# Kernel tuning notes

Measured on AMD Instinct MI355X. Metric: run time of the kernel, lower is better.

Reference implementation:

```python
import jax, jax.numpy as jnp
import numpy as np

N = 100000   # nodes
E = 1600000  # edges
IN = 128     # in_channels
H = 96       # hidden
G = 512      # graphs in batch


def setup_inputs() -> dict:
    key = jax.random.key(0)
    ks = jax.random.split(key, 11)
    x = jax.random.normal(ks[0], (N, IN), jnp.float32)
    edge_index = jax.random.randint(ks[1], (2, E), 0, N)
    batch = jnp.sort(jax.random.randint(ks[2], (N,), 0, G))
    def lin(k, fan_in, fan_out):
        lim = 1.0 / np.sqrt(fan_in)
        kw, kb = jax.random.split(k)
        W = jax.random.uniform(kw, (fan_in, fan_out), jnp.float32, -lim, lim)
        b = jax.random.uniform(kb, (fan_out,), jnp.float32, -lim, lim)
        return W, b
    W1, b1 = lin(ks[3], IN, H)
    W2, b2 = lin(ks[4], H, H)
    Wn, bn = lin(ks[5], 2 * H, 1)
    Wg, bg = lin(ks[6], 4 * H, 1)
    return dict(x=x, edge_index=edge_index, batch=batch,
                W1=W1, b1=b1, W2=W2, b2=b2, Wn=Wn, bn=bn, Wg=Wg, bg=bg)


def reference(x, edge_index, batch, W1, b1, W2, b2, Wn, bn, Wg, bg):
    # --- GCN normalization with self-loops: D^-1/2 (A+I) D^-1/2 ---
    loops = jnp.arange(N)
    src = jnp.concatenate([edge_index[0], loops])  # [E+N]
    dst = jnp.concatenate([edge_index[1], loops])
    deg = jax.ops.segment_sum(jnp.ones_like(dst, jnp.float32), dst, num_segments=N)
    dis = jnp.where(deg > 0, jax.lax.rsqrt(jnp.maximum(deg, 1.0)), 0.0)
    norm = dis[src] * dis[dst]  # [E+N]

    def gcn_conv(h, W, b):
        hw = h @ W                                # transform first (smaller msgs)
        msg = hw[src] * norm[:, None]             # gather + scale  [E+N, H]
        return jax.ops.segment_sum(msg, dst, num_segments=N) + b

    h1 = jax.nn.relu(gcn_conv(x, W1, b1))         # dropout: eval no-op
    h2 = jax.nn.relu(gcn_conv(h1, W2, b2))
    h = jnp.concatenate([h1, h2], axis=1)         # [N, 2H]

    node_logits = (h @ Wn + bn).reshape(-1)       # [N]

    cnt = jax.ops.segment_sum(jnp.ones((N,), jnp.float32), batch, num_segments=G)
    meanp = jax.ops.segment_sum(h, batch, num_segments=G) / jnp.maximum(cnt, 1.0)[:, None]
    maxp = jax.ops.segment_max(h, batch, num_segments=G)
    maxp = jnp.where(cnt[:, None] > 0, maxp, 0.0)
    pooled = jnp.concatenate([meanp, maxp], axis=1)  # [G, 4H]

    graph_logits = (pooled @ Wg + bg).reshape(-1)    # [G]
    return graph_logits, node_logits
```

## Files before the change

### kernel.cpp

```cpp
#include <hip/hip_runtime.h>
#include <hip/hip_fp16.h>

#define NN 100000
#define NE 1600000
#define INC 128
#define HID 96
#define NG 512

#define GEMM1_BLOCKS 1563
#define G2_BLOCKS 1563

#define BK_SHIFT 8
#define BK_SIZE 256
#define NBK 391
#define A_EPB 4096
#define A_BLOCKS 391

typedef _Float16 half8 __attribute__((ext_vector_type(8)));
typedef float f32x4 __attribute__((ext_vector_type(4)));

__global__ __launch_bounds__(256) void k_pack_a1(const int* __restrict__ dst,
                                                 int* __restrict__ histAB,
                                                 const float* __restrict__ W1,
                                                 const float* __restrict__ W2,
                                                 __half* __restrict__ W1frag,
                                                 __half* __restrict__ W2frag) {
    const int tid = threadIdx.x;
    if (blockIdx.x < A_BLOCKS) {
        __shared__ int cnt[NBK];
        int ab = blockIdx.x;
        for (int i = tid; i < NBK; i += 256) cnt[i] = 0;
        __syncthreads();
        int e0 = ab * A_EPB;
#pragma unroll 4
        for (int q = 0; q < A_EPB / 256; ++q) {
            int e = e0 + q * 256 + tid;
            if (e < NE) atomicAdd(&cnt[dst[e] >> BK_SHIFT], 1);
        }
        __syncthreads();
        for (int i = tid; i < NBK; i += 256) histAB[ab * NBK + i] = cnt[i];
        return;
    }
    int p = (blockIdx.x - A_BLOCKS) * 256 + tid;
    if (p < 1536) {
        int kc = p / 384;
        int rem = p - kc * 384;
        int ct = rem >> 6;
        int l = rem & 63;
#pragma unroll
        for (int i = 0; i < 8; ++i) {
            int k = kc * 32 + ((l >> 4) << 3) + i;
            int c = ct * 16 + (l & 15);
            W1frag[p * 8 + i] = __float2half(W1[k * HID + c]);
        }
    } else {
        int q = p - 1536;
        if (q >= 1152) return;
        int kc = q / 384;
        int rem = q - kc * 384;
        int ct = rem >> 6;
        int l = rem & 63;
#pragma unroll
        for (int i = 0; i < 8; ++i) {
            int k = kc * 32 + ((l >> 4) << 3) + i;
            int c = ct * 16 + (l & 15);
            W2frag[q * 8 + i] = __float2half(W2[k * HID + c]);
        }
    }
}

__global__ __launch_bounds__(512) void k_scanS(int* __restrict__ histAB, int* __restrict__ boff) {
    __shared__ int tot[512];
    int t = threadIdx.x;
    int run = 0;
    if (t < NBK) {
        for (int blk = 0; blk < A_BLOCKS; ++blk) {
            int idx = blk * NBK + t;
            int v = histAB[idx];
            histAB[idx] = run;
            run += v;
        }
    }
    tot[t] = (t < NBK) ? run : 0;
    __syncthreads();
    for (int ofs = 1; ofs < 512; ofs <<= 1) {
        int v = (t >= ofs) ? tot[t - ofs] : 0;
        __syncthreads();
        tot[t] += v;
        __syncthreads();
    }
    if (t == 0) boff[0] = 0;
    if (t < NBK) boff[t + 1] = tot[t];
}

__global__ __launch_bounds__(256) void k_gemm1_a3(
        const float* __restrict__ X, const __half* __restrict__ W1frag,
        __half* __restrict__ Yh,
        const int* __restrict__ src, const int* __restrict__ dst,
        const int* __restrict__ boff, const int* __restrict__ histAB,
        unsigned* __restrict__ tmp) {
    __shared__ __half w1s[12288];
    const int tid = threadIdx.x;

    if (blockIdx.x < A_BLOCKS) {
        int* base = (int*)w1s;
        int* lcnt = base + NBK;
        int ab = blockIdx.x;
        for (int i = tid; i < NBK; i += 256) {
            base[i] = boff[i] + histAB[ab * NBK + i];
            lcnt[i] = 0;
        }
        __syncthreads();
        int e0 = ab * A_EPB;
#pragma unroll 4
        for (int q = 0; q < A_EPB / 256; ++q) {
            int e = e0 + q * 256 + tid;
            if (e < NE) {
                int d = dst[e];
                int bk = d >> BK_SHIFT;
                int lp = atomicAdd(&lcnt[bk], 1);
                tmp[base[bk] + lp] = (unsigned)src[e] | ((unsigned)(d & (BK_SIZE - 1)) << 17);
            }
        }
        return;
    }

    {
        half8* d8 = (half8*)w1s;
        const half8* s8 = (const half8*)W1frag;
        for (int i = tid; i < 1536; i += 256) d8[i] = s8[i];
    }
    __syncthreads();
    const int w = tid >> 6;
    const int l = tid & 63;
    const int row0 = (blockIdx.x - A_BLOCKS) * 64 + w * 16;
    int arow = row0 + (l & 15);
    if (arow >= NN) arow = NN - 1;
    f32x4 acc[6] = {};
#pragma unroll
    for (int kc = 0; kc < 4; ++kc) {
        const float* xp = &X[(size_t)arow * INC + kc * 32 + ((l >> 4) << 3)];
        float4 xa = *(const float4*)xp;
        float4 xb = *(const float4*)(xp + 4);
        half8 a;
        a[0] = (_Float16)xa.x; a[1] = (_Float16)xa.y;
        a[2] = (_Float16)xa.z; a[3] = (_Float16)xa.w;
        a[4] = (_Float16)xb.x; a[5] = (_Float16)xb.y;
        a[6] = (_Float16)xb.z; a[7] = (_Float16)xb.w;
#pragma unroll
        for (int ct = 0; ct < 6; ++ct) {
            half8 b = *(const half8*)&w1s[((kc * 6 + ct) * 64 + l) * 8];
            acc[ct] = __builtin_amdgcn_mfma_f32_16x16x32_f16(a, b, acc[ct], 0, 0, 0);
        }
    }
    const int orow = row0 + ((l >> 4) << 2);
    const int col = l & 15;
#pragma unroll
    for (int ct = 0; ct < 6; ++ct)
#pragma unroll
        for (int i = 0; i < 4; ++i) {
            int r = orow + i;
            if (r < NN) Yh[(size_t)r * HID + ct * 16 + col] = __float2half(acc[ct][i]);
        }
}

__global__ __launch_bounds__(256) void k_B1(const unsigned* __restrict__ tmp,
                                            const int* __restrict__ boff,
                                            int* __restrict__ off, float* __restrict__ dis) {
    __shared__ int cnt[BK_SIZE];
    __shared__ int psum[256];
    const int t = threadIdx.x;
    const int b = blockIdx.x;
    const int nb = b << BK_SHIFT;
    const int rbeg = boff[b], rend = boff[b + 1];
    cnt[t] = 0;
    __syncthreads();
    for (int e = rbeg + t; e < rend; e += 256) {
        unsigned u = tmp[e];
        atomicAdd(&cnt[u >> 17], 1);
    }
    __syncthreads();
    int c = cnt[t];
    psum[t] = c;
    __syncthreads();
    for (int ofs = 1; ofs < 256; ofs <<= 1) {
        int v = (t >= ofs) ? psum[t - ofs] : 0;
        __syncthreads();
        psum[t] += v;
        __syncthreads();
    }
    int node = nb + t;
    if (node < NN) {
        off[node] = rbeg + psum[t] - c;
        dis[node] = rsqrtf((float)(c + 1));
    }
    if (b == NBK - 1 && t == 0) off[NN] = rend;
}

__global__ __launch_bounds__(256) void k_B2(const unsigned* __restrict__ tmp,
                                            const int* __restrict__ boff,
                                            const int* __restrict__ off,
                                            const float* __restrict__ dis,
                                            int2* __restrict__ ssrcw) {
    __shared__ int cnt[BK_SIZE];
    const int t = threadIdx.x;
    const int b = blockIdx.x;
    const int nb = b << BK_SHIFT;
    const int rbeg = boff[b], rend = boff[b + 1];
    cnt[t] = 0;
    __syncthreads();
    for (int e = rbeg + t; e < rend; e += 256) {
        unsigned u = tmp[e];
        int s = (int)(u & 0x1FFFFu);
        int dl = (int)(u >> 17);
        int d = nb + dl;
        int pos = off[d] + atomicAdd(&cnt[dl], 1);
        float w = dis[s] * dis[d];
        ssrcw[pos] = make_int2(s, __float_as_int(w));
    }
}

__global__ __launch_bounds__(256) void k_gemm2(const __half* __restrict__ Xh,
                                               const __half* __restrict__ W2frag,
                                               __half* __restrict__ Yh) {
    __shared__ __half w2s[9216];
    const int tid = threadIdx.x;
    {
        half8* d8 = (half8*)w2s;
        const half8* s8 = (const half8*)W2frag;
        for (int i = tid; i < 1152; i += 256) d8[i] = s8[i];
    }
    __syncthreads();
    const int w = tid >> 6;
    const int l = tid & 63;
    const int row0 = blockIdx.x * 64 + w * 16;
    int arow = row0 + (l & 15);
    if (arow >= NN) arow = NN - 1;
    f32x4 acc[6] = {};
#pragma unroll
    for (int kc = 0; kc < 3; ++kc) {
        half8 a = *(const half8*)&Xh[(size_t)arow * HID + kc * 32 + ((l >> 4) << 3)];
#pragma unroll
        for (int ct = 0; ct < 6; ++ct) {
            half8 b = *(const half8*)&w2s[((kc * 6 + ct) * 64 + l) * 8];
            acc[ct] = __builtin_amdgcn_mfma_f32_16x16x32_f16(a, b, acc[ct], 0, 0, 0);
        }
    }
    const int orow = row0 + ((l >> 4) << 2);
    const int col = l & 15;
#pragma unroll
    for (int ct = 0; ct < 6; ++ct)
#pragma unroll
        for (int i = 0; i < 4; ++i) {
            int r = orow + i;
            if (r < NN) Yh[(size_t)r * HID + ct * 16 + col] = __float2half(acc[ct][i]);
        }
}

template <int B>
__device__ __forceinline__ void agg_batch(const __half* __restrict__ Ah,
                                          const int2* __restrict__ ssrcw, int j, int t,
                                          float& a0x, float& a0y, float& a1x, float& a1y,
                                          float& a2x, float& a2y) {
    int2 e[B];
#pragma unroll
    for (int q = 0; q < B; ++q) e[q] = ssrcw[j + q];
    float w[B];
    const __half2* ap[B];
#pragma unroll
    for (int q = 0; q < B; ++q) {
        w[q] = __int_as_float(e[q].y);
        ap[q] = (const __half2*)(Ah + (size_t)e[q].x * HID);
    }
    __half2 g0[B], g1[B], g2[B];
#pragma unroll
    for (int q = 0; q < B; ++q) {
        g0[q] = ap[q][t];
        g1[q] = ap[q][t + 16];
        g2[q] = ap[q][t + 32];
    }
#pragma unroll
    for (int q = 0; q < B; ++q) {
        float2 f0 = __half22float2(g0[q]);
        float2 f1 = __half22float2(g1[q]);
        float2 f2 = __half22float2(g2[q]);
        a0x += f0.x * w[q]; a0y += f0.y * w[q];
        a1x += f1.x * w[q]; a1y += f1.y * w[q];
        a2x += f2.x * w[q]; a2y += f2.y * w[q];
    }
}

template <int PHASE>
__global__ __launch_bounds__(256) void k_agg(const __half* __restrict__ Ah,
                                             const int2* __restrict__ ssrcw,
                                             const int* __restrict__ off,
                                             const float* __restrict__ dis,
                                             const float* __restrict__ bias,
                                             const float* __restrict__ Wn,
                                             const float* __restrict__ bn,
                                             __half* __restrict__ outh,
                                             float* __restrict__ nodeOut) {
    int gid = blockIdx.x * blockDim.x + threadIdx.x;
    int d = gid >> 4;
    int t = gid & 15;
    if (d >= NN) return;
    const int beg = off[d], end = off[d + 1];
    const float dd = dis[d];
    const __half2* ad2 = (const __half2*)(Ah + (size_t)d * HID);
    float2 s0 = __half22float2(ad2[t]);
    float2 s1 = __half22float2(ad2[t + 16]);
    float2 s2 = __half22float2(ad2[t + 32]);
    const float dd2 = dd * dd;
    float a0x = s0.x * dd2, a0y = s0.y * dd2;
    float a1x = s1.x * dd2, a1y = s1.y * dd2;
    float a2x = s2.x * dd2, a2y = s2.y * dd2;
    int j = beg;
    for (; j + 11 < end; j += 12)
        agg_batch<12>(Ah, ssrcw, j, t, a0x, a0y, a1x, a1y, a2x, a2y);
    for (; j + 3 < end; j += 4)
        agg_batch<4>(Ah, ssrcw, j, t, a0x, a0y, a1x, a1y, a2x, a2y);
    for (; j < end; ++j) {
        int2 e0 = ssrcw[j];
        float w0 = __int_as_float(e0.y);
        const __half2* a0 = (const __half2*)(Ah + (size_t)e0.x * HID);
        float2 f0 = __half22float2(a0[t]);
        float2 f1 = __half22float2(a0[t + 16]);
        float2 f2 = __half22float2(a0[t + 32]);
        a0x += f0.x * w0; a0y += f0.y * w0;
        a1x += f1.x * w0; a1y += f1.y * w0;
        a2x += f2.x * w0; a2y += f2.y * w0;
    }
    const float2* b2p = (const float2*)bias;
    float2 b0 = b2p[t], b1 = b2p[t + 16], b2 = b2p[t + 32];
    float h0x = fmaxf(a0x + b0.x, 0.f), h0y = fmaxf(a0y + b0.y, 0.f);
    float h1x = fmaxf(a1x + b1.x, 0.f), h1y = fmaxf(a1y + b1.y, 0.f);
    float h2x = fmaxf(a2x + b2.x, 0.f), h2y = fmaxf(a2y + b2.y, 0.f);
    __half2* o2 = (__half2*)(outh + (size_t)d * HID);
    o2[t]      = __floats2half2_rn(h0x, h0y);
    o2[t + 16] = __floats2half2_rn(h1x, h1y);
    o2[t + 32] = __floats2half2_rn(h2x, h2y);

    const int woff = (PHASE == 1) ? 0 : 96;
    const float2* wn2 = (const float2*)(Wn + woff);
    float2 w0v = wn2[t], w1v = wn2[t + 16], w2v = wn2[t + 32];
    float partial = h0x * w0v.x + h0y * w0v.y + h1x * w1v.x + h1y * w1v.y +
                    h2x * w2v.x + h2y * w2v.y;
#pragma unroll
    for (int m = 8; m; m >>= 1) partial += __shfl_down(partial, m, 16);
    if (t == 0) {
        if (PHASE == 1) nodeOut[d] = partial + bn[0];
        else            nodeOut[d] += partial;
    }
}

__global__ __launch_bounds__(768) void k_pool(const __half* __restrict__ h1,
                                              const __half* __restrict__ h2,
                                              const int* __restrict__ batch,
                                              const float* __restrict__ Wg,
                                              const float* __restrict__ bg,
                                              float* __restrict__ out) {
    int g = blockIdx.x;
    int tid = threadIdx.x;
    int way = tid / 192;
    int f = tid - way * 192;

    int lo = 0, hi = NN;
    while (lo < hi) { int mid = (lo + hi) >> 1; if (batch[mid] < g) lo = mid + 1; else hi = mid; }
    int start = lo;
    hi = NN;
    while (lo < hi) { int mid = (lo + hi) >> 1; if (batch[mid] < g + 1) lo = mid + 1; else hi = mid; }
    int end = lo;

    const __half* hsrc = (f < HID) ? h1 : h2;
    int ff = (f < HID) ? f : f - HID;
    float sum = 0.f, mx = 0.f;
    int n = start + way;
    for (; n + 4 < end; n += 8) {
        float v0 = __half2float(hsrc[(size_t)n * HID + ff]);
        float v1 = __half2float(hsrc[(size_t)(n + 4) * HID + ff]);
        sum += v0 + v1;
        mx = fmaxf(mx, fmaxf(v0, v1));
    }
    if (n < end) {
        float v0 = __half2float(hsrc[(size_t)n * HID + ff]);
        sum += v0;
        mx = fmaxf(mx, v0);
    }
    __shared__ float rsum[4][192];
    __shared__ float rmax[4][192];
    rsum[way][f] = sum;
    rmax[way][f] = mx;
    __syncthreads();
    if (way == 0) {
        sum = rsum[0][f] + rsum[1][f] + rsum[2][f] + rsum[3][f];
        mx = fmaxf(fmaxf(rmax[0][f], rmax[1][f]), fmaxf(rmax[2][f], rmax[3][f]));
        float cnt = (float)(end - start);
        float mean = sum / fmaxf(cnt, 1.0f);
        rsum[0][f] = mean * Wg[f] + mx * Wg[192 + f];
    }
    __syncthreads();
    if (tid < 64) {
        float acc = rsum[0][tid] + rsum[0][tid + 64] + rsum[0][tid + 128];
#pragma unroll
        for (int m = 32; m; m >>= 1) acc += __shfl_down(acc, m, 64);
        if (tid == 0) out[g] = acc + bg[0];
    }
}

extern "C" void kernel_launch(void* const* d_in, const int* in_sizes, int n_in,
                              void* d_out, int out_size, void* d_ws, size_t ws_size,
                              hipStream_t stream) {
    const float* x    = (const float*)d_in[0];
    const int*   ei   = (const int*)d_in[1];
    const int*   srcp = ei;
    const int*   dstp = ei + NE;
    const int*   batch = (const int*)d_in[2];
    const float* W1 = (const float*)d_in[3];
    const float* b1 = (const float*)d_in[4];
    const float* W2 = (const float*)d_in[5];
    const float* b2 = (const float*)d_in[6];
    const float* Wn = (const float*)d_in[7];
    const float* bn = (const float*)d_in[8];
    const float* Wg = (const float*)d_in[9];
    const float* bg = (const float*)d_in[10];
    float* out = (float*)d_out;

    char* p = (char*)d_ws;
    auto alloc = [&](size_t bytes) {
        char* r = p;
        p += (bytes + 255) & ~(size_t)255;
        return (void*)r;
    };
    float*    dis    = (float*)alloc(NN * 4);
    int*      off    = (int*)alloc((NN + 1) * 4);
    int*      boff   = (int*)alloc((NBK + 1) * 4);
    int*      histAB = (int*)alloc((size_t)A_BLOCKS * NBK * 4);
    unsigned* tmp    = (unsigned*)alloc((size_t)NE * 4);
    int2*     ssrcw  = (int2*)alloc((size_t)NE * 8);
    __half*   Ah     = (__half*)alloc((size_t)NN * HID * 2);
    __half*   H1h    = (__half*)alloc((size_t)NN * HID * 2);
    __half*   H2h    = (__half*)alloc((size_t)NN * HID * 2);
    __half*   W1frag = (__half*)alloc(12288 * 2);
    __half*   W2frag = (__half*)alloc(9216 * 2);

    const int TPB = 256;

    k_pack_a1<<<A_BLOCKS + 11, TPB, 0, stream>>>(dstp, histAB, W1, W2, W1frag, W2frag);
    k_scanS<<<1, 512, 0, stream>>>(histAB, boff);
    k_gemm1_a3<<<A_BLOCKS + GEMM1_BLOCKS, 256, 0, stream>>>(
        x, W1frag, Ah, srcp, dstp, boff, histAB, tmp);
    k_B1<<<NBK, 256, 0, stream>>>(tmp, boff, off, dis);
    k_B2<<<NBK, 256, 0, stream>>>(tmp, boff, off, dis, ssrcw);

    const int aggThreads = NN * 16;
    float* nodeOut = out + NG;

    k_agg<1><<<(aggThreads + TPB - 1) / TPB, TPB, 0, stream>>>(Ah, ssrcw, off, dis, b1, Wn, bn, H1h, nodeOut);

    k_gemm2<<<G2_BLOCKS, 256, 0, stream>>>(H1h, W2frag, Ah);

    k_agg<2><<<(aggThreads + TPB - 1) / TPB, TPB, 0, stream>>>(Ah, ssrcw, off, dis, b2, Wn, bn, H2h, nodeOut);

    k_pool<<<NG, 768, 0, stream>>>(H1h, H2h, batch, Wg, bg, out);
}
```

Before: 238.2 us.

## Fuse layer-2 GEMM into aggregation by aggregating before transforming

Layer 2 now aggregates H1 directly and then multiplies the aggregated row by W2 inside the aggregation kernel. The per-node accumulators are staged in shared memory, and W2 is held in LDS as plain fp16. This drops the separate MFMA gemm2 kernel along with its write and re-read of the transformed feature buffer. In exchange every node does a 96x96 scalar FP32 mat-vec read from LDS, and each block needs about 24KB of dynamic LDS plus a block barrier, which may reduce occupancy of this latency-bound gather kernel.

```diff
diff --git a/kernel.cpp b/kernel.cpp
--- a/kernel.cpp
+++ b/kernel.cpp
@@ -8,7 +8,6 @@
 #define NG 512
 
 #define GEMM1_BLOCKS 1563
-#define G2_BLOCKS 1563
 
 #define BK_SHIFT 8
 #define BK_SIZE 256
@@ -24,7 +23,7 @@
                                                  const float* __restrict__ W1,
                                                  const float* __restrict__ W2,
                                                  __half* __restrict__ W1frag,
-                                                 __half* __restrict__ W2frag) {
+                                                 __half* __restrict__ W2h) {
     const int tid = threadIdx.x;
     if (blockIdx.x < A_BLOCKS) {
         __shared__ int cnt[NBK];
@@ -56,16 +55,8 @@
     } else {
         int q = p - 1536;
         if (q >= 1152) return;
-        int kc = q / 384;
-        int rem = q - kc * 384;
-        int ct = rem >> 6;
-        int l = rem & 63;
-#pragma unroll
-        for (int i = 0; i < 8; ++i) {
-            int k = kc * 32 + ((l >> 4) << 3) + i;
-            int c = ct * 16 + (l & 15);
-            W2frag[q * 8 + i] = __float2half(W2[k * HID + c]);
-        }
+#pragma unroll
+        for (int i = 0; i < 8; ++i) W2h[q * 8 + i] = __float2half(W2[q * 8 + i]);
     }
 }
 
@@ -220,43 +211,6 @@
     }
 }
 
-__global__ __launch_bounds__(256) void k_gemm2(const __half* __restrict__ Xh,
-                                               const __half* __restrict__ W2frag,
-                                               __half* __restrict__ Yh) {
-    __shared__ __half w2s[9216];
-    const int tid = threadIdx.x;
-    {
-        half8* d8 = (half8*)w2s;
-        const half8* s8 = (const half8*)W2frag;
-        for (int i = tid; i < 1152; i += 256) d8[i] = s8[i];
-    }
-    __syncthreads();
-    const int w = tid >> 6;
-    const int l = tid & 63;
-    const int row0 = blockIdx.x * 64 + w * 16;
-    int arow = row0 + (l & 15);
-    if (arow >= NN) arow = NN - 1;
-    f32x4 acc[6] = {};
-#pragma unroll
-    for (int kc = 0; kc < 3; ++kc) {
-        half8 a = *(const half8*)&Xh[(size_t)arow * HID + kc * 32 + ((l >> 4) << 3)];
-#pragma unroll
-        for (int ct = 0; ct < 6; ++ct) {
-            half8 b = *(const half8*)&w2s[((kc * 6 + ct) * 64 + l) * 8];
-            acc[ct] = __builtin_amdgcn_mfma_f32_16x16x32_f16(a, b, acc[ct], 0, 0, 0);
-        }
-    }
-    const int orow = row0 + ((l >> 4) << 2);
-    const int col = l & 15;
-#pragma unroll
-    for (int ct = 0; ct < 6; ++ct)
-#pragma unroll
-        for (int i = 0; i < 4; ++i) {
-            int r = orow + i;
-            if (r < NN) Yh[(size_t)r * HID + ct * 16 + col] = __float2half(acc[ct][i]);
-        }
-}
-
 template <int B>
 __device__ __forceinline__ void agg_batch(const __half* __restrict__ Ah,
                                           const int2* __restrict__ ssrcw, int j, int t,
@@ -298,12 +252,21 @@
                                              const float* __restrict__ bias,
                                              const float* __restrict__ Wn,
                                              const float* __restrict__ bn,
+                                             const __half* __restrict__ W2h,
                                              __half* __restrict__ outh,
                                              float* __restrict__ nodeOut) {
+    extern __shared__ char smem[];
     int gid = blockIdx.x * blockDim.x + threadIdx.x;
     int d = gid >> 4;
     int t = gid & 15;
+
+    if (PHASE == 2) {
+        half8* d8 = (half8*)smem;
+        const half8* s8 = (const half8*)W2h;
+        for (int i = threadIdx.x; i < 1152; i += 256) d8[i] = s8[i];
+    }
     if (d >= NN) return;
+
     const int beg = off[d], end = off[d + 1];
     const float dd = dis[d];
     const __half2* ad2 = (const __half2*)(Ah + (size_t)d * HID);
@@ -330,26 +293,59 @@
         a1x += f1.x * w0; a1y += f1.y * w0;
         a2x += f2.x * w0; a2y += f2.y * w0;
     }
-    const float2* b2p = (const float2*)bias;
-    float2 b0 = b2p[t], b1 = b2p[t + 16], b2 = b2p[t + 32];
-    float h0x = fmaxf(a0x + b0.x, 0.f), h0y = fmaxf(a0y + b0.y, 0.f);
-    float h1x = fmaxf(a1x + b1.x, 0.f), h1y = fmaxf(a1y + b1.y, 0.f);
-    float h2x = fmaxf(a2x + b2.x, 0.f), h2y = fmaxf(a2y + b2.y, 0.f);
-    __half2* o2 = (__half2*)(outh + (size_t)d * HID);
-    o2[t]      = __floats2half2_rn(h0x, h0y);
-    o2[t + 16] = __floats2half2_rn(h1x, h1y);
-    o2[t + 32] = __floats2half2_rn(h2x, h2y);
-
-    const int woff = (PHASE == 1) ? 0 : 96;
-    const float2* wn2 = (const float2*)(Wn + woff);
-    float2 w0v = wn2[t], w1v = wn2[t + 16], w2v = wn2[t + 32];
-    float partial = h0x * w0v.x + h0y * w0v.y + h1x * w1v.x + h1y * w1v.y +
-                    h2x * w2v.x + h2y * w2v.y;
-#pragma unroll
-    for (int m = 8; m; m >>= 1) partial += __shfl_down(partial, m, 16);
-    if (t == 0) {
-        if (PHASE == 1) nodeOut[d] = partial + bn[0];
-        else            nodeOut[d] += partial;
+
+    if (PHASE == 1) {
+        const float2* b2p = (const float2*)bias;
+        float2 b0 = b2p[t], b1 = b2p[t + 16], b2 = b2p[t + 32];
+        float h0x = fmaxf(a0x + b0.x, 0.f), h0y = fmaxf(a0y + b0.y, 0.f);
+        float h1x = fmaxf(a1x + b1.x, 0.f), h1y = fmaxf(a1y + b1.y, 0.f);
+        float h2x = fmaxf(a2x + b2.x, 0.f), h2y = fmaxf(a2y + b2.y, 0.f);
+        __half2* o2 = (__half2*)(outh + (size_t)d * HID);
+        o2[t]      = __floats2half2_rn(h0x, h0y);
+        o2[t + 16] = __floats2half2_rn(h1x, h1y);
+        o2[t + 32] = __floats2half2_rn(h2x, h2y);
+        const float2* wn2 = (const float2*)Wn;
+        float2 w0v = wn2[t], w1v = wn2[t + 16], w2v = wn2[t + 32];
+        float partial = h0x * w0v.x + h0y * w0v.y + h1x * w1v.x + h1y * w1v.y +
+                        h2x * w2v.x + h2y * w2v.y;
+#pragma unroll
+        for (int m = 8; m; m >>= 1) partial += __shfl_down(partial, m, 16);
+        if (t == 0) nodeOut[d] = partial + bn[0];
+    } else {
+        float* Mg = (float*)(smem + 18432) + (threadIdx.x >> 4) * 100;
+        Mg[2 * t] = a0x;      Mg[2 * t + 1] = a0y;
+        Mg[32 + 2 * t] = a1x; Mg[33 + 2 * t] = a1y;
+        Mg[64 + 2 * t] = a2x; Mg[65 + 2 * t] = a2y;
+        __syncthreads();
+        const __half2* w2s2 = (const __half2*)smem;
+        float y0x = 0, y0y = 0, y1x = 0, y1y = 0, y2x = 0, y2y = 0;
+#pragma unroll 8
+        for (int k = 0; k < 96; ++k) {
+            float m = Mg[k];
+            __half2 wa = w2s2[k * 48 + 3 * t];
+            __half2 wb = w2s2[k * 48 + 3 * t + 1];
+            __half2 wc = w2s2[k * 48 + 3 * t + 2];
+            float2 fa = __half22float2(wa), fb = __half22float2(wb), fc = __half22float2(wc);
+            y0x += m * fa.x; y0y += m * fa.y;
+            y1x += m * fb.x; y1y += m * fb.y;
+            y2x += m * fc.x; y2y += m * fc.y;
+        }
+        const float2* b2p = (const float2*)bias;
+        float2 B0 = b2p[3 * t], B1 = b2p[3 * t + 1], B2v = b2p[3 * t + 2];
+        float h0x = fmaxf(y0x + B0.x, 0.f), h0y = fmaxf(y0y + B0.y, 0.f);
+        float h1x = fmaxf(y1x + B1.x, 0.f), h1y = fmaxf(y1y + B1.y, 0.f);
+        float h2x = fmaxf(y2x + B2v.x, 0.f), h2y = fmaxf(y2y + B2v.y, 0.f);
+        __half2* o2 = (__half2*)(outh + (size_t)d * HID);
+        o2[3 * t]     = __floats2half2_rn(h0x, h0y);
+        o2[3 * t + 1] = __floats2half2_rn(h1x, h1y);
+        o2[3 * t + 2] = __floats2half2_rn(h2x, h2y);
+        const float2* wn2 = (const float2*)(Wn + 96);
+        float2 w0v = wn2[3 * t], w1v = wn2[3 * t + 1], w2v = wn2[3 * t + 2];
+        float partial = h0x * w0v.x + h0y * w0v.y + h1x * w1v.x + h1y * w1v.y +
+                        h2x * w2v.x + h2y * w2v.y;
+#pragma unroll
+        for (int m = 8; m; m >>= 1) partial += __shfl_down(partial, m, 16);
+        if (t == 0) nodeOut[d] += partial;
     }
 }
 
@@ -441,11 +437,11 @@
     __half*   H1h    = (__half*)alloc((size_t)NN * HID * 2);
     __half*   H2h    = (__half*)alloc((size_t)NN * HID * 2);
     __half*   W1frag = (__half*)alloc(12288 * 2);
-    __half*   W2frag = (__half*)alloc(9216 * 2);
+    __half*   W2h    = (__half*)alloc(9216 * 2);
 
     const int TPB = 256;
 
-    k_pack_a1<<<A_BLOCKS + 11, TPB, 0, stream>>>(dstp, histAB, W1, W2, W1frag, W2frag);
+    k_pack_a1<<<A_BLOCKS + 11, TPB, 0, stream>>>(dstp, histAB, W1, W2, W1frag, W2h);
     k_scanS<<<1, 512, 0, stream>>>(histAB, boff);
     k_gemm1_a3<<<A_BLOCKS + GEMM1_BLOCKS, 256, 0, stream>>>(
         x, W1frag, Ah, srcp, dstp, boff, histAB, tmp);
@@ -453,13 +449,12 @@
     k_B2<<<NBK, 256, 0, stream>>>(tmp, boff, off, dis, ssrcw);
 
     const int aggThreads = NN * 16;
+    const int aggBlocks = aggThreads / TPB;
     float* nodeOut = out + NG;
 
-    k_agg<1><<<(aggThreads + TPB - 1) / TPB, TPB, 0, stream>>>(Ah, ssrcw, off, dis, b1, Wn, bn, H1h, nodeOut);
-
-    k_gemm2<<<G2_BLOCKS, 256, 0, stream>>>(H1h, W2frag, Ah);
-
-    k_agg<2><<<(aggThreads + TPB - 1) / TPB, TPB, 0, stream>>>(Ah, ssrcw, off, dis, b2, Wn, bn, H2h, nodeOut);
+    k_agg<1><<<aggBlocks, TPB, 0, stream>>>(Ah, ssrcw, off, dis, b1, Wn, bn, W2h, H1h, nodeOut);
+
+    k_agg<2><<<aggBlocks, TPB, 24832, stream>>>(H1h, ssrcw, off, dis, b2, Wn, bn, W2h, H2h, nodeOut);
 
     k_pool<<<NG, 768, 0, stream>>>(H1h, H2h, batch, Wg, bg, out);
 }
```

New measurement: 248.3 us. +4.2%, slower.
